# Optimization experiments

Hardware: AMD Instinct MI355X
Metric: run time of the kernel (lower is better)

Reference implementation:

```python
import jax, jax.numpy as jnp
from jax import lax
import numpy as np

B, N, K = 8, 4096, 64          # clouds, points per cloud, max neighbors
N1, N2 = N // 2, N // 8        # fps ratio 0.5, then 0.25
R1, R2 = 0.2, 0.4              # ball-query radii


def setup_inputs() -> dict:
    key = jax.random.key(0)
    ks = jax.random.split(key, 7)
    def w(k, i, o):
        return jax.random.normal(k, (i, o), jnp.float32) / np.sqrt(i).astype(np.float32)
    return {
        "pos": jax.random.uniform(ks[0], (B, N, 3), jnp.float32),
        "w1a": w(ks[1], 3, 64),    "b1a": jnp.zeros(64, jnp.float32),
        "w1b": w(ks[2], 64, 64),   "b1b": jnp.zeros(64, jnp.float32),
        "w2a": w(ks[3], 67, 128),  "b2a": jnp.zeros(128, jnp.float32),
        "w2b": w(ks[4], 128, 128), "b2b": jnp.zeros(128, jnp.float32),
        "w3a": w(ks[5], 131, 256), "b3a": jnp.zeros(256, jnp.float32),
        "w3b": w(ks[6], 256, 1024),"b3b": jnp.zeros(1024, jnp.float32),
    }


def fps(pos, n_samples):
    # farthest point sampling, deterministic start at index 0. pos: [n, 3]
    d0 = jnp.sum((pos - pos[0]) ** 2, axis=-1)
    def step(mind, _):
        nxt = jnp.argmax(mind)
        d = jnp.sum((pos - pos[nxt]) ** 2, axis=-1)
        return jnp.minimum(mind, d), nxt
    _, idxs = lax.scan(step, d0, None, length=n_samples - 1)
    return jnp.concatenate([jnp.zeros((1,), idxs.dtype), idxs])


def ball_query(centers, pts, r):
    # up to K neighbors within radius r (nearest-first); centers are a subset of pts
    d2 = jnp.sum((centers[:, None, :] - pts[None, :, :]) ** 2, axis=-1)  # [M, n]
    neg = jnp.where(d2 <= r * r, -d2, -jnp.inf)
    vals, nbr = lax.top_k(neg, K)
    return nbr, vals > -jnp.inf  # [M, K] indices, validity mask


def mlp(x, w1, b1, w2, b2, relu_last):
    h = jax.nn.relu(x @ w1 + b1) @ w2 + b2
    return jax.nn.relu(h) if relu_last else h


def masked_max(h, mask):
    # max over neighbor axis; every center has itself as a valid neighbor
    return jnp.max(jnp.where(mask[..., None], h, -jnp.inf), axis=1)


def reference(pos, w1a, b1a, w1b, b1b, w2a, b2a, w2b, b2b, w3a, b3a, w3b, b3b):
    def single(p):  # p: [N, 3]
        # SA1: x is None -> per-edge input is relative position only
        idx1 = fps(p, N1)
        c1 = p[idx1]                                   # [N1, 3]
        nbr1, m1 = ball_query(c1, p, R1)               # [N1, K]
        rel1 = p[nbr1] - c1[:, None, :]                # [N1, K, 3]
        x1 = masked_max(mlp(rel1, w1a, b1a, w1b, b1b, True), m1)   # [N1, 64]
        # SA2: per-edge input is [x_j, pos_j - pos_i]
        idx2 = fps(c1, N2)
        c2 = c1[idx2]                                  # [N2, 3]
        nbr2, m2 = ball_query(c2, c1, R2)              # [N2, K]
        feat2 = jnp.concatenate([x1[nbr2], c1[nbr2] - c2[:, None, :]], axis=-1)  # [N2,K,67]
        x2 = masked_max(mlp(feat2, w2a, b2a, w2b, b2b, True), m2)  # [N2, 128]
        # Global SA: MLP on [x, pos] then global max pool
        g = mlp(jnp.concatenate([x2, c2], axis=-1), w3a, b3a, w3b, b3b, False)   # [N2,1024]
        return jnp.max(g, axis=0)                      # [1024]
    return jax.vmap(single)(pos)                       # [B, 1024]
```

## Files before the change

kernel.cpp:

```cpp
#include <hip/hip_runtime.h>
#include <cstdint>
#include <cstddef>


static constexpr int Bc = 8;
static constexpr int Np = 4096;
static constexpr int Kn = 64;
static constexpr int M1 = 2048;
static constexpr int M2 = 512;
static constexpr int LDX = 132;

#define DEVINL __device__ __forceinline__

DEVINL float d2_exact(float ax, float ay, float az, float bx, float by, float bz) {
    float dx = __fsub_rn(ax, bx);
    float dy = __fsub_rn(ay, by);
    float dz = __fsub_rn(az, bz);
    float xx = __fmul_rn(dx, dx);
    float yy = __fmul_rn(dy, dy);
    float zz = __fmul_rn(dz, dz);
    return __fadd_rn(__fadd_rn(xx, yy), zz);
}

template <int CTRL, int RM, int BM>
DEVINL unsigned long long dpp_max_step(unsigned long long k) {
    unsigned lo = (unsigned)k, hi = (unsigned)(k >> 32);
    unsigned slo = (unsigned)__builtin_amdgcn_update_dpp(0, (int)lo, CTRL, RM, BM, true);
    unsigned shi = (unsigned)__builtin_amdgcn_update_dpp(0, (int)hi, CTRL, RM, BM, true);
    unsigned long long s = ((unsigned long long)shi << 32) | (unsigned long long)slo;
    return s > k ? s : k;
}

DEVINL unsigned long long wave_max_u64_dpp(unsigned long long k) {
    k = dpp_max_step<0x111, 0xf, 0xf>(k);
    k = dpp_max_step<0x112, 0xf, 0xf>(k);
    k = dpp_max_step<0x114, 0xf, 0xf>(k);
    k = dpp_max_step<0x118, 0xf, 0xf>(k);
    k = dpp_max_step<0x142, 0xa, 0xf>(k);
    k = dpp_max_step<0x143, 0xc, 0xf>(k);
    return k;
}

__global__ __launch_bounds__(512)
void fps2x_kernel(const float* __restrict__ pos, float* __restrict__ c1,
                  float* __restrict__ c2, float* __restrict__ X) {
    constexpr int NT = 512;
    __shared__ float sc[Np * 3];
    __shared__ float s2c[M1 * 3];
    __shared__ unsigned long long slots[3];
    const int b = blockIdx.x;
    const int t = threadIdx.x;
    const int lane = t & 63;

    {
        constexpr int PT = Np / NT;
        const float* base = pos + (size_t)b * Np * 3;
        float px[PT], py[PT], pz[PT], mind[PT];
        #pragma unroll
        for (int j = 0; j < PT; ++j) {
            int p = j * NT + t;
            px[j] = base[p * 3 + 0];
            py[j] = base[p * 3 + 1];
            pz[j] = base[p * 3 + 2];
            sc[p * 3 + 0] = px[j];
            sc[p * 3 + 1] = py[j];
            sc[p * 3 + 2] = pz[j];
        }
        if (t == 0) { slots[0] = 0; slots[1] = 0; slots[2] = 0; }
        float x0 = base[0], y0 = base[1], z0 = base[2];
        __syncthreads();

        float bv = -1.0f; int bi = 0;
        #pragma unroll
        for (int j = 0; j < PT; ++j) {
            float d = d2_exact(px[j], py[j], pz[j], x0, y0, z0);
            mind[j] = d;
            if (d > bv) { bv = d; bi = j * NT + t; }
        }
        unsigned long long key = ((unsigned long long)__float_as_uint(bv) << 32)
                               | (unsigned long long)(0xFFFFFFFFu - (unsigned)bi);
        key = wave_max_u64_dpp(key);
        if (lane == 63) atomicMax(&slots[1], key);
        if (t == 0) {
            c1[((size_t)b * M1) * 3 + 0] = x0;
            c1[((size_t)b * M1) * 3 + 1] = y0;
            c1[((size_t)b * M1) * 3 + 2] = z0;
            s2c[0] = x0; s2c[1] = y0; s2c[2] = z0;
        }
        int rd = 1, wr = 2, rs = 0;
        for (int s = 1; s < M1; ++s) {
            __syncthreads();
            unsigned long long km = slots[rd];
            if (t == 0) slots[rs] = 0;
            int idx = (int)(0xFFFFFFFFu - (unsigned)km);
            float cx = sc[idx * 3 + 0];
            float cy = sc[idx * 3 + 1];
            float cz = sc[idx * 3 + 2];
            if (t == 0) {
                c1[((size_t)b * M1 + s) * 3 + 0] = cx;
                c1[((size_t)b * M1 + s) * 3 + 1] = cy;
                c1[((size_t)b * M1 + s) * 3 + 2] = cz;
                s2c[s * 3 + 0] = cx; s2c[s * 3 + 1] = cy; s2c[s * 3 + 2] = cz;
            }
            bv = -1.0f; bi = 0;
            #pragma unroll
            for (int j = 0; j < PT; ++j) {
                float d = d2_exact(px[j], py[j], pz[j], cx, cy, cz);
                float m = fminf(mind[j], d);
                mind[j] = m;
                if (m > bv) { bv = m; bi = j * NT + t; }
            }
            key = ((unsigned long long)__float_as_uint(bv) << 32)
                | (unsigned long long)(0xFFFFFFFFu - (unsigned)bi);
            key = wave_max_u64_dpp(key);
            if (lane == 63) atomicMax(&slots[wr], key);
            int nrd = wr; wr = rs; rs = rd; rd = nrd;
        }
    }
    __syncthreads();
    if (t == 0) { slots[0] = 0; slots[1] = 0; slots[2] = 0; }
    __syncthreads();

    {
        constexpr int PT = M1 / NT;
        float px[PT], py[PT], pz[PT], mind[PT];
        #pragma unroll
        for (int j = 0; j < PT; ++j) {
            int p = j * NT + t;
            px[j] = s2c[p * 3 + 0];
            py[j] = s2c[p * 3 + 1];
            pz[j] = s2c[p * 3 + 2];
        }
        float x0 = s2c[0], y0 = s2c[1], z0 = s2c[2];
        float bv = -1.0f; int bi = 0;
        #pragma unroll
        for (int j = 0; j < PT; ++j) {
            float d = d2_exact(px[j], py[j], pz[j], x0, y0, z0);
            mind[j] = d;
            if (d > bv) { bv = d; bi = j * NT + t; }
        }
        unsigned long long key = ((unsigned long long)__float_as_uint(bv) << 32)
                               | (unsigned long long)(0xFFFFFFFFu - (unsigned)bi);
        key = wave_max_u64_dpp(key);
        if (lane == 63) atomicMax(&slots[1], key);
        if (t == 0) {
            c2[((size_t)b * M2) * 3 + 0] = x0;
            c2[((size_t)b * M2) * 3 + 1] = y0;
            c2[((size_t)b * M2) * 3 + 2] = z0;
            float* xr = X + (size_t)(b * M2) * LDX;
            xr[128] = x0; xr[129] = y0; xr[130] = z0;
        }
        int rd = 1, wr = 2, rs = 0;
        for (int s = 1; s < M2; ++s) {
            __syncthreads();
            unsigned long long km = slots[rd];
            if (t == 0) slots[rs] = 0;
            int idx = (int)(0xFFFFFFFFu - (unsigned)km);
            float cx = s2c[idx * 3 + 0];
            float cy = s2c[idx * 3 + 1];
            float cz = s2c[idx * 3 + 2];
            if (t == 0) {
                c2[((size_t)b * M2 + s) * 3 + 0] = cx;
                c2[((size_t)b * M2 + s) * 3 + 1] = cy;
                c2[((size_t)b * M2 + s) * 3 + 2] = cz;
                float* xr = X + (size_t)(b * M2 + s) * LDX;
                xr[128] = cx; xr[129] = cy; xr[130] = cz;
            }
            bv = -1.0f; bi = 0;
            #pragma unroll
            for (int j = 0; j < PT; ++j) {
                float d = d2_exact(px[j], py[j], pz[j], cx, cy, cz);
                float m = fminf(mind[j], d);
                mind[j] = m;
                if (m > bv) { bv = m; bi = j * NT + t; }
            }
            key = ((unsigned long long)__float_as_uint(bv) << 32)
                | (unsigned long long)(0xFFFFFFFFu - (unsigned)bi);
            key = wave_max_u64_dpp(key);
            if (lane == 63) atomicMax(&slots[wr], key);
            int nrd = wr; wr = rs; rs = rd; rd = nrd;
        }
    }
}

template <int NPT>
__global__ __launch_bounds__(256)
void bq_kernel(const float* __restrict__ pts, const float* __restrict__ ctr,
               int mshift, float r2, int* __restrict__ nbr) {
    constexpr int CH = NPT / 64;
    constexpr int CAP = 1024;
    __shared__ uint2 cbuf[4][CAP];
    const int lane = threadIdx.x & 63;
    const int wl = threadIdx.x >> 6;
    int w = __builtin_amdgcn_readfirstlane((int)(blockIdx.x * 4 + wl));
    const int b = w >> mshift;
    const float* pb = pts + (size_t)b * NPT * 3;
    const float* cp = ctr + (size_t)w * 3;
    float cx = cp[0], cy = cp[1], cz = cp[2];
    const unsigned r2b = __float_as_uint(r2);

    unsigned ub[CH];
    int cnt = 0;
    #pragma unroll
    for (int j = 0; j < CH; ++j) {
        int p = j * 64 + lane;
        float d = d2_exact(pb[p * 3 + 0], pb[p * 3 + 1], pb[p * 3 + 2], cx, cy, cz);
        ub[j] = __float_as_uint(d);
        cnt += __popcll(__ballot(ub[j] <= r2b));
    }
    int* out = nbr + (size_t)w * Kn;
    const unsigned long long lml = (1ull << lane) - 1ull;

    if (cnt <= Kn) {
        int basep = 0;
        #pragma unroll
        for (int j = 0; j < CH; ++j) {
            bool v = ub[j] <= r2b;
            unsigned long long mk = __ballot(v);
            if (v) out[basep + __popcll(mk & lml)] = j * 64 + lane;
            basep += __popcll(mk);
        }
        if (lane >= cnt) out[lane] = -1;
    } else if (cnt <= CAP) {
        uint2* buf = cbuf[wl];
        int basep = 0;
        #pragma unroll
        for (int j = 0; j < CH; ++j) {
            bool v = ub[j] <= r2b;
            unsigned long long mk = __ballot(v);
            if (v) buf[basep + __popcll(mk & lml)] =
                       make_uint2(ub[j], (unsigned)(j * 64 + lane));
            basep += __popcll(mk);
        }
        const int C2 = (cnt + 63) >> 6;
        unsigned cb[CAP / 64], ci[CAP / 64];
        #pragma unroll
        for (int e = 0; e < CAP / 64; ++e) {
            if (e >= C2) break;
            int p = e * 64 + lane;
            uint2 v = buf[p];
            cb[e] = (p < cnt) ? v.x : 0xFFFFFFFFu;
            ci[e] = v.y;
        }
        unsigned lo = 0, hi = r2b;
        while (lo < hi) {
            unsigned mid = lo + ((hi - lo) >> 1);
            int c = 0;
            #pragma unroll
            for (int e = 0; e < CAP / 64; ++e) {
                if (e >= C2) break;
                c += __popcll(__ballot(cb[e] <= mid));
            }
            if (c >= Kn) hi = mid; else lo = mid + 1;
        }
        const unsigned tt = lo;
        int cntLess = 0;
        #pragma unroll
        for (int e = 0; e < CAP / 64; ++e) {
            if (e >= C2) break;
            cntLess += __popcll(__ballot(cb[e] < tt));
        }
        const int quota = Kn - cntLess;
        int baseLt = 0, eqseen = 0;
        #pragma unroll
        for (int e = 0; e < CAP / 64; ++e) {
            if (e >= C2) break;
            bool lt = cb[e] < tt;
            bool eq = cb[e] == tt;
            unsigned long long mlt = __ballot(lt);
            unsigned long long meq = __ballot(eq);
            if (lt) out[baseLt + __popcll(mlt & lml)] = (int)ci[e];
            if (eq) {
                int rr = eqseen + __popcll(meq & lml);
                if (rr < quota) out[cntLess + rr] = (int)ci[e];
            }
            baseLt += __popcll(mlt);
            eqseen += __popcll(meq);
        }
    } else {
        unsigned lo = 0, hi = r2b;
        while (lo < hi) {
            unsigned mid = lo + ((hi - lo) >> 1);
            int c = 0;
            #pragma unroll
            for (int j = 0; j < CH; ++j) c += __popcll(__ballot(ub[j] <= mid));
            if (c >= Kn) hi = mid; else lo = mid + 1;
        }
        const unsigned tt = lo;
        int cntLess = 0;
        #pragma unroll
        for (int j = 0; j < CH; ++j) cntLess += __popcll(__ballot(ub[j] < tt));
        const int quota = Kn - cntLess;
        int baseLt = 0, eqseen = 0;
        #pragma unroll
        for (int j = 0; j < CH; ++j) {
            bool lt = ub[j] < tt;
            bool eq = ub[j] == tt;
            unsigned long long mlt = __ballot(lt);
            unsigned long long meq = __ballot(eq);
            if (lt) out[baseLt + __popcll(mlt & lml)] = j * 64 + lane;
            if (eq) {
                int rr = eqseen + __popcll(meq & lml);
                if (rr < quota) out[cntLess + rr] = j * 64 + lane;
            }
            baseLt += __popcll(mlt);
            eqseen += __popcll(meq);
        }
    }
}

__global__ __launch_bounds__(256)
void mlp1_kernel(const float* __restrict__ pos, const float* __restrict__ c1,
                 const int* __restrict__ nbr, const float* __restrict__ w1aT,
                 const float* __restrict__ w1bT, const float* __restrict__ b1b,
                 float* __restrict__ x1) {
    const int lane = threadIdx.x & 63;
    int w = __builtin_amdgcn_readfirstlane((int)(blockIdx.x * 4 + (threadIdx.x >> 6)));
    const int b = w >> 11;
    const int ii = nbr[(size_t)w * Kn + lane];
    const bool valid = ii >= 0;
    const int i2 = valid ? ii : 0;
    const float* pp = pos + ((size_t)b * Np + i2) * 3;
    const float* cc = c1 + (size_t)w * 3;
    float rx = pp[0] - cc[0], ry = pp[1] - cc[1], rz = pp[2] - cc[2];
    float h1[64];
    #pragma unroll
    for (int h = 0; h < 64; ++h) {
        float4 wv = ((const float4*)w1aT)[h];
        float a = fmaf(rx, wv.x, fmaf(ry, wv.y, fmaf(rz, wv.z, wv.w)));
        h1[h] = fmaxf(a, 0.0f);
    }
    float* orow = x1 + (size_t)w * 64;
    for (int c4 = 0; c4 < 16; ++c4) {
        float v4[4];
        #pragma unroll
        for (int cq = 0; cq < 4; ++cq) {
            int c = c4 * 4 + cq;
            float acc = b1b[c];
            const float4* wr = (const float4*)(w1bT + (size_t)c * 64);
            #pragma unroll
            for (int q = 0; q < 16; ++q) {
                float4 wv = wr[q];
                acc = fmaf(h1[4 * q + 0], wv.x, acc);
                acc = fmaf(h1[4 * q + 1], wv.y, acc);
                acc = fmaf(h1[4 * q + 2], wv.z, acc);
                acc = fmaf(h1[4 * q + 3], wv.w, acc);
            }
            float v = fmaxf(acc, 0.0f);
            v = valid ? v : -__builtin_inff();
            #pragma unroll
            for (int o = 32; o > 0; o >>= 1) v = fmaxf(v, __shfl_xor(v, o, 64));
            v4[cq] = v;
        }
        if (lane == 0)
            ((float4*)orow)[c4] = make_float4(v4[0], v4[1], v4[2], v4[3]);
    }
}

__global__ __launch_bounds__(256)
void mlp2_kernel(const float* __restrict__ x1, const float* __restrict__ c1,
                 const float* __restrict__ c2, const int* __restrict__ nbr2,
                 const float* __restrict__ w2aT, const float* __restrict__ w2bT,
                 const float* __restrict__ b2b, float* __restrict__ X) {
    const int lane = threadIdx.x & 63;
    int w = __builtin_amdgcn_readfirstlane((int)(blockIdx.x * 4 + (threadIdx.x >> 6)));
    const int b = w >> 9;
    const int ii = nbr2[(size_t)w * Kn + lane];
    const bool valid = ii >= 0;
    const int i2 = valid ? ii : 0;

    float x[68];
    const float4* xr = (const float4*)(x1 + ((size_t)b * M1 + i2) * 64);
    #pragma unroll
    for (int q = 0; q < 16; ++q) {
        float4 v = xr[q];
        x[4 * q + 0] = v.x; x[4 * q + 1] = v.y;
        x[4 * q + 2] = v.z; x[4 * q + 3] = v.w;
    }
    const float* cc = c2 + (size_t)w * 3;
    const float* cp = c1 + ((size_t)b * M1 + i2) * 3;
    x[64] = cp[0] - cc[0];
    x[65] = cp[1] - cc[1];
    x[66] = cp[2] - cc[2];
    x[67] = 0.0f;

    float h1[128];
    #pragma unroll
    for (int h = 0; h < 128; ++h) {
        const float4* r4 = (const float4*)(w2aT + (size_t)h * 80);
        float acc = 0.0f;
        #pragma unroll
        for (int q = 0; q < 16; ++q) {
            float4 wv = r4[q];
            acc = fmaf(x[4 * q + 0], wv.x, acc);
            acc = fmaf(x[4 * q + 1], wv.y, acc);
            acc = fmaf(x[4 * q + 2], wv.z, acc);
            acc = fmaf(x[4 * q + 3], wv.w, acc);
        }
        float4 tl = r4[16];
        acc = fmaf(x[64], tl.x, acc);
        acc = fmaf(x[65], tl.y, acc);
        acc = fmaf(x[66], tl.z, acc);
        acc += tl.w;
        h1[h] = fmaxf(acc, 0.0f);
    }
    float* orow = X + (size_t)w * LDX;
    for (int c4 = 0; c4 < 32; ++c4) {
        float v4[4];
        #pragma unroll
        for (int cq = 0; cq < 4; ++cq) {
            int c = c4 * 4 + cq;
            float acc = b2b[c];
            const float4* wr = (const float4*)(w2bT + (size_t)c * 128);
            #pragma unroll
            for (int q = 0; q < 32; ++q) {
                float4 wv = wr[q];
                acc = fmaf(h1[4 * q + 0], wv.x, acc);
                acc = fmaf(h1[4 * q + 1], wv.y, acc);
                acc = fmaf(h1[4 * q + 2], wv.z, acc);
                acc = fmaf(h1[4 * q + 3], wv.w, acc);
            }
            float v = fmaxf(acc, 0.0f);
            v = valid ? v : -__builtin_inff();
            #pragma unroll
            for (int o = 32; o > 0; o >>= 1) v = fmaxf(v, __shfl_xor(v, o, 64));
            v4[cq] = v;
        }
        if (lane == 0) {
            orow[c4 * 4 + 0] = v4[0]; orow[c4 * 4 + 1] = v4[1];
            orow[c4 * 4 + 2] = v4[2]; orow[c4 * 4 + 3] = v4[3];
        }
    }
}

__global__ __launch_bounds__(256)
void gemm1_kernel(const float* __restrict__ X, const float* __restrict__ w3a,
                  const float* __restrict__ b3a, float* __restrict__ H) {
    const int r = blockIdx.x;
    const int c = threadIdx.x;
    const float* xr = X + (size_t)r * LDX;
    float acc = b3a[c];
    for (int i = 0; i < 131; ++i)
        acc = fmaf(xr[i], w3a[(size_t)i * 256 + c], acc);
    H[(size_t)r * 256 + c] = fmaxf(acc, 0.0f);
}

__global__ __launch_bounds__(256)
void gemm2_kernel(const float* __restrict__ H, const float* __restrict__ w3b,
                  float* __restrict__ part) {
    __shared__ float As[32][33];
    __shared__ float Bs[32][64];
    __shared__ float red[8][64];
    const int bidx = blockIdx.x;
    const int nt = bidx & 15;
    const int mt = (bidx >> 4) & 15;
    const int b = bidx >> 8;
    const int row0 = b * M2 + mt * 32;
    const int col0 = nt * 64;
    const int t = threadIdx.x;
    const int rg = t >> 5, cg = t & 31;

    float acc[4][2] = {{0.f, 0.f}, {0.f, 0.f}, {0.f, 0.f}, {0.f, 0.f}};
    for (int k0 = 0; k0 < 256; k0 += 32) {
        #pragma unroll
        for (int q = 0; q < 4; ++q) {
            int id = t + q * 256;
            As[id >> 5][id & 31] = H[(size_t)(row0 + (id >> 5)) * 256 + k0 + (id & 31)];
        }
        #pragma unroll
        for (int q = 0; q < 8; ++q) {
            int id = t + q * 256;
            Bs[id >> 6][id & 63] = w3b[(size_t)(k0 + (id >> 6)) * 1024 + col0 + (id & 63)];
        }
        __syncthreads();
        #pragma unroll
        for (int kk = 0; kk < 32; ++kk) {
            float b0 = Bs[kk][cg * 2 + 0];
            float b1 = Bs[kk][cg * 2 + 1];
            #pragma unroll
            for (int j = 0; j < 4; ++j) {
                float a = As[rg * 4 + j][kk];
                acc[j][0] = fmaf(a, b0, acc[j][0]);
                acc[j][1] = fmaf(a, b1, acc[j][1]);
            }
        }
        __syncthreads();
    }
    float m0 = fmaxf(fmaxf(acc[0][0], acc[1][0]), fmaxf(acc[2][0], acc[3][0]));
    float m1 = fmaxf(fmaxf(acc[0][1], acc[1][1]), fmaxf(acc[2][1], acc[3][1]));
    red[rg][cg * 2 + 0] = m0;
    red[rg][cg * 2 + 1] = m1;
    __syncthreads();
    if (t < 64) {
        float v = red[0][t];
        #pragma unroll
        for (int q = 1; q < 8; ++q) v = fmaxf(v, red[q][t]);
        part[((size_t)b * 16 + mt) * 1024 + col0 + t] = v;
    }
}

__global__ __launch_bounds__(256)
void rmax_kernel(const float* __restrict__ part, const float* __restrict__ b3b,
                 float* __restrict__ out) {
    int i = blockIdx.x * 256 + threadIdx.x;
    int b = i >> 10, c = i & 1023;
    float v = -__builtin_inff();
    #pragma unroll
    for (int tt = 0; tt < 16; ++tt)
        v = fmaxf(v, part[((size_t)b * 16 + tt) * 1024 + c]);
    out[i] = v + b3b[c];
}

__global__ __launch_bounds__(256)
void prep_kernel(const float* __restrict__ w1a, const float* __restrict__ b1a,
                 const float* __restrict__ w1b, const float* __restrict__ w2a,
                 const float* __restrict__ b2a, const float* __restrict__ w2b,
                 float* __restrict__ w1aT, float* __restrict__ w1bT,
                 float* __restrict__ w2aT, float* __restrict__ w2bT) {
    int i = blockIdx.x * 256 + threadIdx.x;
    if (i < 64 * 4) {
        int h = i >> 2, d = i & 3;
        w1aT[i] = (d < 3) ? w1a[d * 64 + h] : b1a[h];
    }
    if (i < 64 * 64) {
        int c = i >> 6, h = i & 63;
        w1bT[i] = w1b[h * 64 + c];
    }
    if (i < 128 * 80) {
        int h = i / 80, d = i - h * 80;
        w2aT[i] = (d < 67) ? w2a[d * 128 + h] : ((d == 67) ? b2a[h] : 0.0f);
    }
    {
        int c = i >> 7, h = i & 127;
        w2bT[i] = w2b[h * 128 + c];
    }
}

extern "C" void kernel_launch(void* const* d_in, const int* in_sizes, int n_in,
                              void* d_out, int out_size, void* d_ws, size_t ws_size,
                              hipStream_t stream) {
    const float* pos = (const float*)d_in[0];
    const float* w1a = (const float*)d_in[1];
    const float* b1a = (const float*)d_in[2];
    const float* w1b = (const float*)d_in[3];
    const float* b1b = (const float*)d_in[4];
    const float* w2a = (const float*)d_in[5];
    const float* b2a = (const float*)d_in[6];
    const float* w2b = (const float*)d_in[7];
    const float* b2b = (const float*)d_in[8];
    const float* w3a = (const float*)d_in[9];
    const float* b3a = (const float*)d_in[10];
    const float* w3b = (const float*)d_in[11];
    const float* b3b = (const float*)d_in[12];
    float* out = (float*)d_out;

    char* ws = (char*)d_ws;
    size_t off = 0;
    auto alloc = [&](size_t bytes) -> char* {
        char* p = ws + off;
        off += (bytes + 255) & ~(size_t)255;
        return p;
    };
    float* c1   = (float*)alloc(sizeof(float) * Bc * M1 * 3);
    float* c2   = (float*)alloc(sizeof(float) * Bc * M2 * 3);
    int*   nbr1 = (int*)alloc(sizeof(int) * Bc * M1 * Kn);
    int*   nbr2 = (int*)alloc(sizeof(int) * Bc * M2 * Kn);
    float* x1   = (float*)alloc(sizeof(float) * Bc * M1 * 64);
    float* X    = (float*)alloc(sizeof(float) * Bc * M2 * LDX);
    float* H    = (float*)alloc(sizeof(float) * Bc * M2 * 256);
    float* part = (float*)alloc(sizeof(float) * Bc * 16 * 1024);
    float* w1aT = (float*)alloc(sizeof(float) * 64 * 4);
    float* w1bT = (float*)alloc(sizeof(float) * 64 * 64);
    float* w2aT = (float*)alloc(sizeof(float) * 128 * 80);
    float* w2bT = (float*)alloc(sizeof(float) * 128 * 128);

    prep_kernel<<<dim3(64), dim3(256), 0, stream>>>(w1a, b1a, w1b, w2a, b2a, w2b,
                                                    w1aT, w1bT, w2aT, w2bT);
    fps2x_kernel<<<dim3(Bc), dim3(512), 0, stream>>>(pos, c1, c2, X);
    bq_kernel<Np><<<dim3(Bc * M1 / 4), dim3(256), 0, stream>>>(
        pos, c1, 11, (float)(0.2 * 0.2), nbr1);
    mlp1_kernel<<<dim3(Bc * M1 / 4), dim3(256), 0, stream>>>(
        pos, c1, nbr1, w1aT, w1bT, b1b, x1);
    bq_kernel<M1><<<dim3(Bc * M2 / 4), dim3(256), 0, stream>>>(
        c1, c2, 9, (float)(0.4 * 0.4), nbr2);
    mlp2_kernel<<<dim3(Bc * M2 / 4), dim3(256), 0, stream>>>(
        x1, c1, c2, nbr2, w2aT, w2bT, b2b, X);
    gemm1_kernel<<<dim3(Bc * M2), dim3(256), 0, stream>>>(X, w3a, b3a, H);
    gemm2_kernel<<<dim3(Bc * 16 * 16), dim3(256), 0, stream>>>(H, w3b, part);
    rmax_kernel<<<dim3(32), dim3(256), 0, stream>>>(part, b3b, out);
}
```

Before: 2.585 ms.

## Spatially sort FPS points into Morton cells and skip distance updates via bounding boxes

Before both farthest-point-sampling loops, points are bucketed into an 8x8x8 Morton grid with a shared-memory histogram, scan and scatter, so each thread owns a spatially compact run of points. Each thread keeps a bounding box of its points and skips the distance update when the new center is farther from that box than its current max min-distance. If no lane in a wave needs an update, the wave also skips the DPP reduction and resubmits its cached key. Keys are repacked so the original index still breaks ties the same way. This costs extra setup sorting and a float-tolerance pruning test that must never skip a needed update.

```diff
diff --git a/kernel.cpp b/kernel.cpp
--- a/kernel.cpp
+++ b/kernel.cpp
@@ -41,12 +41,37 @@
     return k;
 }
 
+DEVINL unsigned mort3(unsigned v) {
+    return (v & 1u) | ((v & 2u) << 2) | ((v & 4u) << 4);
+}
+
+DEVINL unsigned cell_of(float x, float y, float z) {
+    int ix = (int)(x * 8.0f); ix = ix < 0 ? 0 : (ix > 7 ? 7 : ix);
+    int iy = (int)(y * 8.0f); iy = iy < 0 ? 0 : (iy > 7 ? 7 : iy);
+    int iz = (int)(z * 8.0f); iz = iz < 0 ? 0 : (iz > 7 ? 7 : iz);
+    return mort3((unsigned)ix) | (mort3((unsigned)iy) << 1) | (mort3((unsigned)iz) << 2);
+}
+
+DEVINL unsigned* scan512(unsigned* h0, unsigned* h1, int t) {
+    unsigned* src = h0; unsigned* dst = h1;
+    for (int d = 1; d < 512; d <<= 1) {
+        unsigned v = src[t];
+        if (t >= d) v += src[t - d];
+        dst[t] = v;
+        __syncthreads();
+        unsigned* tmp = src; src = dst; dst = tmp;
+    }
+    return src;
+}
+
 __global__ __launch_bounds__(512)
 void fps2x_kernel(const float* __restrict__ pos, float* __restrict__ c1,
                   float* __restrict__ c2, float* __restrict__ X) {
     constexpr int NT = 512;
-    __shared__ float sc[Np * 3];
+    __shared__ float scx[Np], scy[Np], scz[Np];
+    __shared__ unsigned spk[Np];
     __shared__ float s2c[M1 * 3];
+    __shared__ unsigned h0[512], h1[512];
     __shared__ unsigned long long slots[3];
     const int b = blockIdx.x;
     const int t = threadIdx.x;
@@ -55,32 +80,63 @@
     {
         constexpr int PT = Np / NT;
         const float* base = pos + (size_t)b * Np * 3;
+        float gx[PT], gy[PT], gz[PT];
+        unsigned gc[PT];
+        #pragma unroll
+        for (int j = 0; j < PT; ++j) {
+            int p = j * NT + t;
+            gx[j] = base[p * 3 + 0];
+            gy[j] = base[p * 3 + 1];
+            gz[j] = base[p * 3 + 2];
+            gc[j] = cell_of(gx[j], gy[j], gz[j]);
+        }
+        float x0 = base[0], y0 = base[1], z0 = base[2];
+        h0[t] = 0;
+        if (t == 0) { slots[0] = 0; slots[1] = 0; slots[2] = 0; }
+        __syncthreads();
+        #pragma unroll
+        for (int j = 0; j < PT; ++j) atomicAdd(&h0[gc[j]], 1u);
+        __syncthreads();
+        unsigned cnt = h0[t];
+        unsigned* inc = scan512(h0, h1, t);
+        inc[t] -= cnt;
+        __syncthreads();
+        #pragma unroll
+        for (int j = 0; j < PT; ++j) {
+            unsigned p = atomicAdd(&inc[gc[j]], 1u);
+            scx[p] = gx[j]; scy[p] = gy[j]; scz[p] = gz[j];
+            spk[p] = ((0xFFFu - (unsigned)(j * NT + t)) << 12) | p;
+        }
+        __syncthreads();
+
         float px[PT], py[PT], pz[PT], mind[PT];
-        #pragma unroll
-        for (int j = 0; j < PT; ++j) {
-            int p = j * NT + t;
-            px[j] = base[p * 3 + 0];
-            py[j] = base[p * 3 + 1];
-            pz[j] = base[p * 3 + 2];
-            sc[p * 3 + 0] = px[j];
-            sc[p * 3 + 1] = py[j];
-            sc[p * 3 + 2] = pz[j];
-        }
-        if (t == 0) { slots[0] = 0; slots[1] = 0; slots[2] = 0; }
-        float x0 = base[0], y0 = base[1], z0 = base[2];
-        __syncthreads();
-
-        float bv = -1.0f; int bi = 0;
+        unsigned oi[PT];
+        #pragma unroll
+        for (int j = 0; j < PT; ++j) {
+            int p = t * PT + j;
+            px[j] = scx[p]; py[j] = scy[p]; pz[j] = scz[p];
+            oi[j] = spk[p];
+        }
+        float lox = px[0], hix = px[0], loy = py[0], hiy = py[0], loz = pz[0], hiz = pz[0];
+        #pragma unroll
+        for (int j = 1; j < PT; ++j) {
+            lox = fminf(lox, px[j]); hix = fmaxf(hix, px[j]);
+            loy = fminf(loy, py[j]); hiy = fmaxf(hiy, py[j]);
+            loz = fminf(loz, pz[j]); hiz = fmaxf(hiz, pz[j]);
+        }
+
+        unsigned long long ck = 0;
         #pragma unroll
         for (int j = 0; j < PT; ++j) {
             float d = d2_exact(px[j], py[j], pz[j], x0, y0, z0);
             mind[j] = d;
-            if (d > bv) { bv = d; bi = j * NT + t; }
-        }
-        unsigned long long key = ((unsigned long long)__float_as_uint(bv) << 32)
-                               | (unsigned long long)(0xFFFFFFFFu - (unsigned)bi);
-        key = wave_max_u64_dpp(key);
-        if (lane == 63) atomicMax(&slots[1], key);
+            unsigned long long kj =
+                ((unsigned long long)__float_as_uint(d) << 24) | (unsigned long long)oi[j];
+            if (kj > ck) ck = kj;
+        }
+        float bmax = __uint_as_float((unsigned)(ck >> 24));
+        unsigned long long wkey = wave_max_u64_dpp(ck);
+        if (lane == 63) atomicMax(&slots[1], wkey);
         if (t == 0) {
             c1[((size_t)b * M1) * 3 + 0] = x0;
             c1[((size_t)b * M1) * 3 + 1] = y0;
@@ -92,57 +148,99 @@
             __syncthreads();
             unsigned long long km = slots[rd];
             if (t == 0) slots[rs] = 0;
-            int idx = (int)(0xFFFFFFFFu - (unsigned)km);
-            float cx = sc[idx * 3 + 0];
-            float cy = sc[idx * 3 + 1];
-            float cz = sc[idx * 3 + 2];
+            unsigned spos = (unsigned)km & 0xFFFu;
+            float cx = scx[spos], cy = scy[spos], cz = scz[spos];
             if (t == 0) {
                 c1[((size_t)b * M1 + s) * 3 + 0] = cx;
                 c1[((size_t)b * M1 + s) * 3 + 1] = cy;
                 c1[((size_t)b * M1 + s) * 3 + 2] = cz;
                 s2c[s * 3 + 0] = cx; s2c[s * 3 + 1] = cy; s2c[s * 3 + 2] = cz;
             }
-            bv = -1.0f; bi = 0;
-            #pragma unroll
-            for (int j = 0; j < PT; ++j) {
-                float d = d2_exact(px[j], py[j], pz[j], cx, cy, cz);
-                float m = fminf(mind[j], d);
-                mind[j] = m;
-                if (m > bv) { bv = m; bi = j * NT + t; }
-            }
-            key = ((unsigned long long)__float_as_uint(bv) << 32)
-                | (unsigned long long)(0xFFFFFFFFu - (unsigned)bi);
-            key = wave_max_u64_dpp(key);
-            if (lane == 63) atomicMax(&slots[wr], key);
+            float dxv = fmaxf(fmaxf(lox - cx, cx - hix), 0.0f);
+            float dyv = fmaxf(fmaxf(loy - cy, cy - hiy), 0.0f);
+            float dzv = fmaxf(fmaxf(loz - cz, cz - hiz), 0.0f);
+            float L = dxv * dxv + dyv * dyv + dzv * dzv;
+            bool fire = (L * 0.999f <= bmax);
+            if (fire) {
+                unsigned long long nck = 0;
+                #pragma unroll
+                for (int j = 0; j < PT; ++j) {
+                    float d = d2_exact(px[j], py[j], pz[j], cx, cy, cz);
+                    float m = fminf(mind[j], d);
+                    mind[j] = m;
+                    unsigned long long kj =
+                        ((unsigned long long)__float_as_uint(m) << 24) | (unsigned long long)oi[j];
+                    if (kj > nck) nck = kj;
+                }
+                ck = nck;
+                bmax = __uint_as_float((unsigned)(ck >> 24));
+            }
+            if (__ballot(fire) != 0ull) wkey = wave_max_u64_dpp(ck);
+            if (lane == 63) atomicMax(&slots[wr], wkey);
             int nrd = wr; wr = rs; rs = rd; rd = nrd;
         }
     }
-    __syncthreads();
-    if (t == 0) { slots[0] = 0; slots[1] = 0; slots[2] = 0; }
     __syncthreads();
 
     {
         constexpr int PT = M1 / NT;
+        float gx[PT], gy[PT], gz[PT];
+        unsigned gc[PT];
+        #pragma unroll
+        for (int j = 0; j < PT; ++j) {
+            int p = j * NT + t;
+            gx[j] = s2c[p * 3 + 0];
+            gy[j] = s2c[p * 3 + 1];
+            gz[j] = s2c[p * 3 + 2];
+            gc[j] = cell_of(gx[j], gy[j], gz[j]);
+        }
+        float x0 = s2c[0], y0 = s2c[1], z0 = s2c[2];
+        h0[t] = 0;
+        if (t == 0) { slots[0] = 0; slots[1] = 0; slots[2] = 0; }
+        __syncthreads();
+        #pragma unroll
+        for (int j = 0; j < PT; ++j) atomicAdd(&h0[gc[j]], 1u);
+        __syncthreads();
+        unsigned cnt = h0[t];
+        unsigned* inc = scan512(h0, h1, t);
+        inc[t] -= cnt;
+        __syncthreads();
+        #pragma unroll
+        for (int j = 0; j < PT; ++j) {
+            unsigned p = atomicAdd(&inc[gc[j]], 1u);
+            scx[p] = gx[j]; scy[p] = gy[j]; scz[p] = gz[j];
+            spk[p] = ((0xFFFu - (unsigned)(j * NT + t)) << 12) | p;
+        }
+        __syncthreads();
+
         float px[PT], py[PT], pz[PT], mind[PT];
-        #pragma unroll
-        for (int j = 0; j < PT; ++j) {
-            int p = j * NT + t;
-            px[j] = s2c[p * 3 + 0];
-            py[j] = s2c[p * 3 + 1];
-            pz[j] = s2c[p * 3 + 2];
-        }
-        float x0 = s2c[0], y0 = s2c[1], z0 = s2c[2];
-        float bv = -1.0f; int bi = 0;
+        unsigned oi[PT];
+        #pragma unroll
+        for (int j = 0; j < PT; ++j) {
+            int p = t * PT + j;
+            px[j] = scx[p]; py[j] = scy[p]; pz[j] = scz[p];
+            oi[j] = spk[p];
+        }
+        float lox = px[0], hix = px[0], loy = py[0], hiy = py[0], loz = pz[0], hiz = pz[0];
+        #pragma unroll
+        for (int j = 1; j < PT; ++j) {
+            lox = fminf(lox, px[j]); hix = fmaxf(hix, px[j]);
+            loy = fminf(loy, py[j]); hiy = fmaxf(hiy, py[j]);
+            loz = fminf(loz, pz[j]); hiz = fmaxf(hiz, pz[j]);
+        }
+
+        unsigned long long ck = 0;
         #pragma unroll
         for (int j = 0; j < PT; ++j) {
             float d = d2_exact(px[j], py[j], pz[j], x0, y0, z0);
             mind[j] = d;
-            if (d > bv) { bv = d; bi = j * NT + t; }
-        }
-        unsigned long long key = ((unsigned long long)__float_as_uint(bv) << 32)
-                               | (unsigned long long)(0xFFFFFFFFu - (unsigned)bi);
-        key = wave_max_u64_dpp(key);
-        if (lane == 63) atomicMax(&slots[1], key);
+            unsigned long long kj =
+                ((unsigned long long)__float_as_uint(d) << 24) | (unsigned long long)oi[j];
+            if (kj > ck) ck = kj;
+        }
+        float bmax = __uint_as_float((unsigned)(ck >> 24));
+        unsigned long long wkey = wave_max_u64_dpp(ck);
+        if (lane == 63) atomicMax(&slots[1], wkey);
         if (t == 0) {
             c2[((size_t)b * M2) * 3 + 0] = x0;
             c2[((size_t)b * M2) * 3 + 1] = y0;
@@ -155,10 +253,8 @@
             __syncthreads();
             unsigned long long km = slots[rd];
             if (t == 0) slots[rs] = 0;
-            int idx = (int)(0xFFFFFFFFu - (unsigned)km);
-            float cx = s2c[idx * 3 + 0];
-            float cy = s2c[idx * 3 + 1];
-            float cz = s2c[idx * 3 + 2];
+            unsigned spos = (unsigned)km & 0xFFFu;
+            float cx = scx[spos], cy = scy[spos], cz = scz[spos];
             if (t == 0) {
                 c2[((size_t)b * M2 + s) * 3 + 0] = cx;
                 c2[((size_t)b * M2 + s) * 3 + 1] = cy;
@@ -166,18 +262,27 @@
                 float* xr = X + (size_t)(b * M2 + s) * LDX;
                 xr[128] = cx; xr[129] = cy; xr[130] = cz;
             }
-            bv = -1.0f; bi = 0;
-            #pragma unroll
-            for (int j = 0; j < PT; ++j) {
-                float d = d2_exact(px[j], py[j], pz[j], cx, cy, cz);
-                float m = fminf(mind[j], d);
-                mind[j] = m;
-                if (m > bv) { bv = m; bi = j * NT + t; }
-            }
-            key = ((unsigned long long)__float_as_uint(bv) << 32)
-                | (unsigned long long)(0xFFFFFFFFu - (unsigned)bi);
-            key = wave_max_u64_dpp(key);
-            if (lane == 63) atomicMax(&slots[wr], key);
+            float dxv = fmaxf(fmaxf(lox - cx, cx - hix), 0.0f);
+            float dyv = fmaxf(fmaxf(loy - cy, cy - hiy), 0.0f);
+            float dzv = fmaxf(fmaxf(loz - cz, cz - hiz), 0.0f);
+            float L = dxv * dxv + dyv * dyv + dzv * dzv;
+            bool fire = (L * 0.999f <= bmax);
+            if (fire) {
+                unsigned long long nck = 0;
+                #pragma unroll
+                for (int j = 0; j < PT; ++j) {
+                    float d = d2_exact(px[j], py[j], pz[j], cx, cy, cz);
+                    float m = fminf(mind[j], d);
+                    mind[j] = m;
+                    unsigned long long kj =
+                        ((unsigned long long)__float_as_uint(m) << 24) | (unsigned long long)oi[j];
+                    if (kj > nck) nck = kj;
+                }
+                ck = nck;
+                bmax = __uint_as_float((unsigned)(ck >> 24));
+            }
+            if (__ballot(fire) != 0ull) wkey = wave_max_u64_dpp(ck);
+            if (lane == 63) atomicMax(&slots[wr], wkey);
             int nrd = wr; wr = rs; rs = rd; rd = nrd;
         }
     }
```

Measured after the change: 2.501 ms (median of 4 runs). -3.3%, faster.
